# Optimization experiments

Measured on AMD Instinct MI355X. Metric: run time of the kernel, lower is better.

Reference implementation:

```python
import jax, jax.numpy as jnp
import numpy as np

B, C, E, TARGET = 8, 256, 18000, 4500


def setup_inputs() -> dict:
    key = jax.random.key(0)
    k1, k2 = jax.random.split(key)
    fe = jax.random.normal(k1, (B, C, E), dtype=jnp.float32)
    # group_ids[b, e] = index of the pooled output edge that original edge e
    # was merged into by the union-find during edge collapse.
    group_ids = jax.random.randint(k2, (B, E), 0, TARGET, dtype=jnp.int64)
    return {"fe": fe, "group_ids": group_ids, "target": TARGET}


def reference(fe, group_ids, target):
    # MeshUnion.rebuild_features: out feature of each surviving edge group =
    # mean of features of all original edges merged into that group.
    b, c, e = fe.shape
    # flatten (batch, group) into one segment id so a single segment_sum handles all meshes
    flat_ids = (jnp.arange(b, dtype=group_ids.dtype)[:, None] * target + group_ids).reshape(-1)  # [B*E]
    feats = fe.transpose(0, 2, 1).reshape(b * e, c)  # [B*E, C]
    sums = jax.ops.segment_sum(feats, flat_ids, num_segments=b * target)          # [B*T, C]
    counts = jax.ops.segment_sum(jnp.ones((b * e,), fe.dtype), flat_ids,
                                 num_segments=b * target)                          # [B*T]
    out = sums / jnp.maximum(counts, 1.0)[:, None]
    return out.reshape(b, target, c).transpose(0, 2, 1)  # [B, C, target]
```

## Files before the change

kernel.cpp:

```cpp
#include <hip/hip_runtime.h>

#define BB 8
#define CC 256
#define EE 18000
#define TT 4500
#define BT (BB * TT)
#define BE (BB * EE)
#define W  36
#define S  37
#define NW 500
#define PADDED (NW * S)


__global__ void zero_counts_kernel(int* __restrict__ counts) {
    int i = blockIdx.x * blockDim.x + threadIdx.x;
    if (i < BT) counts[i] = 0;
}

__global__ void count_kernel(const int* __restrict__ gid, int* __restrict__ counts) {
    int i = blockIdx.x * blockDim.x + threadIdx.x;
    if (i < BE) {
        int b = i / EE;
        atomicAdd(&counts[b * TT + gid[i]], 1);
    }
}

__global__ __launch_bounds__(1024) void scan_kernel(const int* __restrict__ counts,
                                                    int* __restrict__ cursor,
                                                    unsigned short* __restrict__ pend16,
                                                    float* __restrict__ inv32) {
    __shared__ int part[1024];
    const int b = blockIdx.x;
    const int t = threadIdx.x;
    const int CHUNK = 5;
    int lo = t * CHUNK; if (lo > TT) lo = TT;
    int hi = lo + CHUNK; if (hi > TT) hi = TT;
    int s = 0;
    for (int i = lo; i < hi; ++i) s += counts[b * TT + i];
    part[t] = s;
    __syncthreads();
    for (int d = 1; d < 1024; d <<= 1) {
        int v = (t >= d) ? part[t - d] : 0;
        __syncthreads();
        part[t] += v;
        __syncthreads();
    }
    int run = part[t] - s;
    for (int i = lo; i < hi; ++i) {
        int cnt = counts[b * TT + i];
        cursor[b * TT + i] = b * EE + run;
        int end = run + cnt;
        pend16[b * TT + i] = (end > 0) ? (unsigned short)((end - 1) + (end - 1) / W) : 0;
        inv32[b * TT + i]  = (cnt > 0) ? 1.0f / (float)cnt : 0.0f;
        run = end;
    }
}

__global__ void scatter_kernel(const int* __restrict__ gid,
                               int* __restrict__ cursor,
                               unsigned short* __restrict__ prank16) {
    int i = blockIdx.x * blockDim.x + threadIdx.x;
    if (i < BE) {
        int b = i / EE;
        int p = atomicAdd(&cursor[b * TT + gid[i]], 1) - b * EE;
        prank16[i] = (unsigned short)(p + p / W);
    }
}


__global__ __launch_bounds__(512, 2) void pool_kernel(const float* __restrict__ fe,
                                                      const unsigned short* __restrict__ prank16,
                                                      const unsigned short* __restrict__ pend16,
                                                      const float* __restrict__ inv32,
                                                      float* __restrict__ out) {
    __shared__ float vals[PADDED];
    __shared__ float part[512];
    const int b   = blockIdx.x >> 8;
    const int c   = blockIdx.x & 255;
    const int tid = threadIdx.x;

    if (tid < NW) vals[S * tid + W] = 0.0f;

    const float4*  fe4 = (const float4*)(fe + (size_t)(b * CC + c) * EE);
    const ushort4* rk4 = (const ushort4*)(prank16 + (size_t)b * EE);
#pragma unroll
    for (int i = 0; i < 9; ++i) {
        int idx = tid + (i << 9);
        if (idx < EE / 4) {
            float4  v = fe4[idx];
            ushort4 r = rk4[idx];
            vals[r.x] = v.x;
            vals[r.y] = v.y;
            vals[r.z] = v.z;
            vals[r.w] = v.w;
        }
    }
    __syncthreads();

    float v[W];
    float sum = 0.0f;
    const int base = S * tid;
    if (tid < NW) {
#pragma unroll
        for (int k = 0; k < W; ++k) { v[k] = vals[base + k]; sum += v[k]; }
    }
    part[tid] = sum;
    __syncthreads();

    if (tid < 64) {
        float ps[8];
        float run = 0.0f;
#pragma unroll
        for (int j = 0; j < 8; ++j) { run += part[tid * 8 + j]; ps[j] = run; }
        float tot = run, sc = run;
#pragma unroll
        for (int d = 1; d < 64; d <<= 1) {
            float o = __shfl_up(sc, d, 64);
            if (tid >= d) sc += o;
        }
        float excl = sc - tot;
#pragma unroll
        for (int j = 0; j < 8; ++j) part[tid * 8 + j] = ps[j] + excl;
    }
    __syncthreads();

    if (tid < NW) {
        float run = (tid > 0) ? part[tid - 1] : 0.0f;
#pragma unroll
        for (int k = 0; k < W; ++k) { run += v[k]; vals[base + k] = run; }
    }
    __syncthreads();

    const unsigned short* pe = pend16 + b * TT;
    const float*          iv = inv32 + b * TT;
    float*                outb = out + (size_t)(b * CC + c) * TT;
#pragma unroll
    for (int k = 0; k < 9; ++k) {
        int g = tid + (k << 9);
        if (g < TT) {
            float Pa = vals[pe[g]];
            float Pb = (g > 0) ? vals[pe[g - 1]] : 0.0f;
            outb[g] = (Pa - Pb) * iv[g];
        }
    }
}

extern "C" void kernel_launch(void* const* d_in, const int* in_sizes, int n_in,
                              void* d_out, int out_size, void* d_ws, size_t ws_size,
                              hipStream_t stream) {
    const float* fe  = (const float*)d_in[0];
    const int*   gid = (const int*)d_in[1];
    float*       out = (float*)d_out;

    int*            counts  = (int*)d_ws;
    int*            cursor  = counts + BT;
    float*          inv32   = (float*)(cursor + BT);
    unsigned short* pend16  = (unsigned short*)(inv32 + BT);
    unsigned short* prank16 = pend16 + BT;

    zero_counts_kernel<<<(BT + 255) / 256, 256, 0, stream>>>(counts);
    count_kernel<<<(BE + 255) / 256, 256, 0, stream>>>(gid, counts);
    scan_kernel<<<BB, 1024, 0, stream>>>(counts, cursor, pend16, inv32);
    scatter_kernel<<<(BE + 255) / 256, 256, 0, stream>>>(gid, cursor, prank16);
    pool_kernel<<<BB * CC, 512, 0, stream>>>(fe, prank16, pend16, inv32, out);
}
```

Baseline: 67.02 us.

## Split segment prefix-sum into two halves to halve shared memory per block

Computes a split point per batch at a group boundary near the middle of the sorted edge order. The pool kernel then processes each half separately with a smaller shared prefix buffer and a warp-shuffle block scan. Smaller LDS usage is meant to allow more resident blocks. In exchange, the fe and rank data are read twice per block, and two extra preprocessing kernels are added.

Result: slower. 100.0 us (+49.3%).

```diff
diff --git a/kernel.cpp b/kernel.cpp
--- a/kernel.cpp
+++ b/kernel.cpp
@@ -6,10 +6,11 @@
 #define TT 4500
 #define BT (BB * TT)
 #define BE (BB * EE)
-#define W  36
-#define S  37
-#define NW 500
-#define PADDED (NW * S)
+#define W  18
+#define SS 19
+#define NW 512
+#define PW (NW * SS)
+#define SP 9000
 
 
 __global__ void zero_counts_kernel(int* __restrict__ counts) {
@@ -26,9 +27,8 @@
 }
 
 __global__ __launch_bounds__(1024) void scan_kernel(const int* __restrict__ counts,
-                                                    int* __restrict__ cursor,
-                                                    unsigned short* __restrict__ pend16,
-                                                    float* __restrict__ inv32) {
+                                                    int* __restrict__ off32,
+                                                    int* __restrict__ cursor) {
     __shared__ int part[1024];
     const int b = blockIdx.x;
     const int t = threadIdx.x;
@@ -47,101 +47,136 @@
     }
     int run = part[t] - s;
     for (int i = lo; i < hi; ++i) {
-        int cnt = counts[b * TT + i];
+        off32[b * TT + i]  = run;
         cursor[b * TT + i] = b * EE + run;
-        int end = run + cnt;
-        pend16[b * TT + i] = (end > 0) ? (unsigned short)((end - 1) + (end - 1) / W) : 0;
-        inv32[b * TT + i]  = (cnt > 0) ? 1.0f / (float)cnt : 0.0f;
-        run = end;
+        run += counts[b * TT + i];
+    }
+}
+
+__global__ __launch_bounds__(512) void split_kernel(const int* __restrict__ off32,
+                                                    int2* __restrict__ split2) {
+    const int b = blockIdx.x;
+    for (int g = threadIdx.x; g < TT; g += 512) {
+        int st = off32[b * TT + g];
+        if (st >= SP && g > 0 && off32[b * TT + g - 1] < SP)
+            split2[b] = make_int2(g, st);
+    }
+}
+
+__global__ void table_kernel(const int* __restrict__ counts,
+                             const int* __restrict__ off32,
+                             const int2* __restrict__ split2,
+                             unsigned short* __restrict__ qa16,
+                             unsigned short* __restrict__ qb16,
+                             float* __restrict__ inv32) {
+    int i = blockIdx.x * blockDim.x + threadIdx.x;
+    if (i < BT) {
+        int b = i / TT;
+        int g = i - b * TT;
+        int2 s2 = split2[b];
+        int st  = off32[i];
+        int cnt = counts[i];
+        int ls  = st - ((g >= s2.x) ? s2.y : 0);
+        int le  = ls + cnt;
+        qa16[i] = cnt ? (unsigned short)((le - 1) + (le - 1) / W + 1) : 0;
+        qb16[i] = ls  ? (unsigned short)((ls - 1) + (ls - 1) / W + 1) : 0;
+        inv32[i] = cnt ? 1.0f / (float)cnt : 0.0f;
     }
 }
 
 __global__ void scatter_kernel(const int* __restrict__ gid,
                                int* __restrict__ cursor,
+                               const int2* __restrict__ split2,
                                unsigned short* __restrict__ prank16) {
     int i = blockIdx.x * blockDim.x + threadIdx.x;
     if (i < BE) {
-        int b = i / EE;
-        int p = atomicAdd(&cursor[b * TT + gid[i]], 1) - b * EE;
-        prank16[i] = (unsigned short)(p + p / W);
-    }
-}
-
-
-__global__ __launch_bounds__(512, 2) void pool_kernel(const float* __restrict__ fe,
-                                                      const unsigned short* __restrict__ prank16,
-                                                      const unsigned short* __restrict__ pend16,
-                                                      const float* __restrict__ inv32,
-                                                      float* __restrict__ out) {
-    __shared__ float vals[PADDED];
-    __shared__ float part[512];
+        int b  = i / EE;
+        int p  = atomicAdd(&cursor[b * TT + gid[i]], 1) - b * EE;
+        int sp = split2[b].y;
+        int h  = (p >= sp) ? 1 : 0;
+        int lp = p - (h ? sp : 0);
+        prank16[i] = (unsigned short)((lp + lp / W) | (h << 15));
+    }
+}
+
+
+__global__ __launch_bounds__(512) void pool_kernel(const float* __restrict__ fe,
+                                                   const unsigned short* __restrict__ prank16,
+                                                   const unsigned short* __restrict__ qa16,
+                                                   const unsigned short* __restrict__ qb16,
+                                                   const float* __restrict__ inv32,
+                                                   const int2* __restrict__ split2,
+                                                   float* __restrict__ out) {
+    __shared__ float vals[PW];
+    __shared__ float wsum[8];
     const int b   = blockIdx.x >> 8;
     const int c   = blockIdx.x & 255;
     const int tid = threadIdx.x;
-
-    if (tid < NW) vals[S * tid + W] = 0.0f;
+    const int wv  = tid >> 6;
+    const int ln  = tid & 63;
 
     const float4*  fe4 = (const float4*)(fe + (size_t)(b * CC + c) * EE);
     const ushort4* rk4 = (const ushort4*)(prank16 + (size_t)b * EE);
-#pragma unroll
-    for (int i = 0; i < 9; ++i) {
-        int idx = tid + (i << 9);
-        if (idx < EE / 4) {
-            float4  v = fe4[idx];
-            ushort4 r = rk4[idx];
-            vals[r.x] = v.x;
-            vals[r.y] = v.y;
-            vals[r.z] = v.z;
-            vals[r.w] = v.w;
-        }
-    }
-    __syncthreads();
-
-    float v[W];
-    float sum = 0.0f;
-    const int base = S * tid;
-    if (tid < NW) {
-#pragma unroll
-        for (int k = 0; k < W; ++k) { v[k] = vals[base + k]; sum += v[k]; }
-    }
-    part[tid] = sum;
-    __syncthreads();
-
-    if (tid < 64) {
-        float ps[8];
-        float run = 0.0f;
-#pragma unroll
-        for (int j = 0; j < 8; ++j) { run += part[tid * 8 + j]; ps[j] = run; }
-        float tot = run, sc = run;
+    const unsigned short* qa = qa16 + b * TT;
+    const unsigned short* qb = qb16 + b * TT;
+    const float*          iv = inv32 + b * TT;
+    float* outb = out + (size_t)(b * CC + c) * TT;
+    const int gs = split2[b].x;
+
+    for (int h = 0; h < 2; ++h) {
+        const int hb = h << 15;
+
+        for (int i = tid; i < PW; i += 512) vals[i] = 0.0f;
+        __syncthreads();
+
+#pragma unroll
+        for (int i = 0; i < 9; ++i) {
+            int idx = tid + (i << 9);
+            if (idx < EE / 4) {
+                float4  v = fe4[idx];
+                ushort4 r = rk4[idx];
+                if ((r.x & 0x8000) == hb) vals[r.x & 0x7fff] = v.x;
+                if ((r.y & 0x8000) == hb) vals[r.y & 0x7fff] = v.y;
+                if ((r.z & 0x8000) == hb) vals[r.z & 0x7fff] = v.z;
+                if ((r.w & 0x8000) == hb) vals[r.w & 0x7fff] = v.w;
+            }
+        }
+        __syncthreads();
+
+        const int base = SS * tid;
+        float sum = 0.0f;
+#pragma unroll
+        for (int k = 0; k < W; ++k) sum += vals[base + k];
+
+        float sc = sum;
 #pragma unroll
         for (int d = 1; d < 64; d <<= 1) {
             float o = __shfl_up(sc, d, 64);
-            if (tid >= d) sc += o;
-        }
-        float excl = sc - tot;
-#pragma unroll
-        for (int j = 0; j < 8; ++j) part[tid * 8 + j] = ps[j] + excl;
-    }
-    __syncthreads();
-
-    if (tid < NW) {
-        float run = (tid > 0) ? part[tid - 1] : 0.0f;
-#pragma unroll
-        for (int k = 0; k < W; ++k) { run += v[k]; vals[base + k] = run; }
-    }
-    __syncthreads();
-
-    const unsigned short* pe = pend16 + b * TT;
-    const float*          iv = inv32 + b * TT;
-    float*                outb = out + (size_t)(b * CC + c) * TT;
-#pragma unroll
-    for (int k = 0; k < 9; ++k) {
-        int g = tid + (k << 9);
-        if (g < TT) {
-            float Pa = vals[pe[g]];
-            float Pb = (g > 0) ? vals[pe[g - 1]] : 0.0f;
+            if (ln >= d) sc += o;
+        }
+        if (ln == 63) wsum[wv] = sc;
+        __syncthreads();
+
+        float cross = 0.0f;
+#pragma unroll
+        for (int j = 0; j < 8; ++j) {
+            float tw = wsum[j];
+            if (j < wv) cross += tw;
+        }
+        float run = cross + (sc - sum);
+#pragma unroll
+        for (int k = 0; k < W; ++k) { run += vals[base + k]; vals[base + k] = run; }
+        __syncthreads();
+
+        const int glo = h ? gs : 0;
+        const int ghi = h ? TT : gs;
+        for (int g = glo + tid; g < ghi; g += 512) {
+            int a = qa[g], bq = qb[g];
+            float Pa = a  ? vals[a - 1]  : 0.0f;
+            float Pb = bq ? vals[bq - 1] : 0.0f;
             outb[g] = (Pa - Pb) * iv[g];
         }
+        __syncthreads();
     }
 }
 
@@ -154,13 +189,18 @@
 
     int*            counts  = (int*)d_ws;
     int*            cursor  = counts + BT;
-    float*          inv32   = (float*)(cursor + BT);
-    unsigned short* pend16  = (unsigned short*)(inv32 + BT);
-    unsigned short* prank16 = pend16 + BT;
+    int*            off32   = cursor + BT;
+    float*          inv32   = (float*)(off32 + BT);
+    unsigned short* qa16    = (unsigned short*)(inv32 + BT);
+    unsigned short* qb16    = qa16 + BT;
+    unsigned short* prank16 = qb16 + BT;
+    int2*           split2  = (int2*)(prank16 + BE);
 
     zero_counts_kernel<<<(BT + 255) / 256, 256, 0, stream>>>(counts);
     count_kernel<<<(BE + 255) / 256, 256, 0, stream>>>(gid, counts);
-    scan_kernel<<<BB, 1024, 0, stream>>>(counts, cursor, pend16, inv32);
-    scatter_kernel<<<(BE + 255) / 256, 256, 0, stream>>>(gid, cursor, prank16);
-    pool_kernel<<<BB * CC, 512, 0, stream>>>(fe, prank16, pend16, inv32, out);
-}
+    scan_kernel<<<BB, 1024, 0, stream>>>(counts, off32, cursor);
+    split_kernel<<<BB, 512, 0, stream>>>(off32, split2);
+    table_kernel<<<(BT + 255) / 256, 256, 0, stream>>>(counts, off32, split2, qa16, qb16, inv32);
+    scatter_kernel<<<(BE + 255) / 256, 256, 0, stream>>>(gid, cursor, split2, prank16);
+    pool_kernel<<<BB * CC, 512, 0, stream>>>(fe, prank16, qa16, qb16, inv32, split2, out);
+}
```

## Use 1024-thread pool blocks with wave-shuffle scan and packed index table

Applied to the files above, without the earlier changes.

The pool kernel now runs 1024 threads per block, each handling 18 padded slots instead of 36. The block scan uses per-wave shuffles plus a 16-entry cross-wave sum instead of a serial 64-thread pass. The scan kernel now writes a packed uint2 table holding both prefix endpoints and the reciprocal count. This removes the neighbour pend lookup and one of the separate loads in the output phase. The aim is to keep every thread busy, drop a barrier and cut per-thread register and serial work. The risks are the 1024-thread block shape and an aggressive launch bound that may force register spilling.

New measurement: 65.88 us. No clear change (-1.7%).

```diff
diff --git a/kernel.cpp b/kernel.cpp
--- a/kernel.cpp
+++ b/kernel.cpp
@@ -6,10 +6,10 @@
 #define TT 4500
 #define BT (BB * TT)
 #define BE (BB * EE)
-#define W  36
-#define S  37
-#define NW 500
-#define PADDED (NW * S)
+#define W  18
+#define SS 19
+#define NT 1024
+#define PW (NT * SS)
 
 
 __global__ void zero_counts_kernel(int* __restrict__ counts) {
@@ -27,8 +27,7 @@
 
 __global__ __launch_bounds__(1024) void scan_kernel(const int* __restrict__ counts,
                                                     int* __restrict__ cursor,
-                                                    unsigned short* __restrict__ pend16,
-                                                    float* __restrict__ inv32) {
+                                                    uint2* __restrict__ tab) {
     __shared__ int part[1024];
     const int b = blockIdx.x;
     const int t = threadIdx.x;
@@ -49,10 +48,12 @@
     for (int i = lo; i < hi; ++i) {
         int cnt = counts[b * TT + i];
         cursor[b * TT + i] = b * EE + run;
-        int end = run + cnt;
-        pend16[b * TT + i] = (end > 0) ? (unsigned short)((end - 1) + (end - 1) / W) : 0;
-        inv32[b * TT + i]  = (cnt > 0) ? 1.0f / (float)cnt : 0.0f;
-        run = end;
+        int en = run + cnt;
+        unsigned int qa = cnt ? (unsigned int)((en - 1) + (en - 1) / W + 1) : 0u;
+        unsigned int qb = run ? (unsigned int)((run - 1) + (run - 1) / W + 1) : 0u;
+        float inv = cnt ? 1.0f / (float)cnt : 0.0f;
+        tab[b * TT + i] = make_uint2(qa | (qb << 16), __float_as_uint(inv));
+        run = en;
     }
 }
 
@@ -68,24 +69,23 @@
 }
 
 
-__global__ __launch_bounds__(512, 2) void pool_kernel(const float* __restrict__ fe,
-                                                      const unsigned short* __restrict__ prank16,
-                                                      const unsigned short* __restrict__ pend16,
-                                                      const float* __restrict__ inv32,
-                                                      float* __restrict__ out) {
-    __shared__ float vals[PADDED];
-    __shared__ float part[512];
+__global__ __launch_bounds__(1024, 8) void pool_kernel(const float* __restrict__ fe,
+                                                       const unsigned short* __restrict__ prank16,
+                                                       const uint2* __restrict__ tab,
+                                                       float* __restrict__ out) {
+    __shared__ float vals[PW];
+    __shared__ float wsum[16];
     const int b   = blockIdx.x >> 8;
     const int c   = blockIdx.x & 255;
     const int tid = threadIdx.x;
-
-    if (tid < NW) vals[S * tid + W] = 0.0f;
+    const int wv  = tid >> 6;
+    const int ln  = tid & 63;
 
     const float4*  fe4 = (const float4*)(fe + (size_t)(b * CC + c) * EE);
     const ushort4* rk4 = (const ushort4*)(prank16 + (size_t)b * EE);
 #pragma unroll
-    for (int i = 0; i < 9; ++i) {
-        int idx = tid + (i << 9);
+    for (int i = 0; i < 5; ++i) {
+        int idx = tid + (i << 10);
         if (idx < EE / 4) {
             float4  v = fe4[idx];
             ushort4 r = rk4[idx];
@@ -97,50 +97,51 @@
     }
     __syncthreads();
 
+    const int base = SS * tid;
     float v[W];
-    float sum = 0.0f;
-    const int base = S * tid;
-    if (tid < NW) {
+    float s0 = 0.0f, s1 = 0.0f;
 #pragma unroll
-        for (int k = 0; k < W; ++k) { v[k] = vals[base + k]; sum += v[k]; }
+    for (int k = 0; k < 9; ++k)  { v[k] = vals[base + k]; s0 += v[k]; }
+#pragma unroll
+    for (int k = 9; k < 18; ++k) { v[k] = vals[base + k]; s1 += v[k]; }
+    const float sum = s0 + s1;
+
+    float sc = sum;
+#pragma unroll
+    for (int d = 1; d < 64; d <<= 1) {
+        float o = __shfl_up(sc, d, 64);
+        if (ln >= d) sc += o;
     }
-    part[tid] = sum;
+    if (ln == 63) wsum[wv] = sc;
     __syncthreads();
 
-    if (tid < 64) {
-        float ps[8];
-        float run = 0.0f;
+    float cross = 0.0f;
 #pragma unroll
-        for (int j = 0; j < 8; ++j) { run += part[tid * 8 + j]; ps[j] = run; }
-        float tot = run, sc = run;
+    for (int j = 0; j < 16; ++j) {
+        float tw = wsum[j];
+        if (j < wv) cross += tw;
+    }
+
+    float run0 = cross + (sc - sum);
+    float run1 = run0 + s0;
 #pragma unroll
-        for (int d = 1; d < 64; d <<= 1) {
-            float o = __shfl_up(sc, d, 64);
-            if (tid >= d) sc += o;
-        }
-        float excl = sc - tot;
+    for (int k = 0; k < 9; ++k)  { run0 += v[k]; vals[base + k] = run0; }
 #pragma unroll
-        for (int j = 0; j < 8; ++j) part[tid * 8 + j] = ps[j] + excl;
-    }
+    for (int k = 9; k < 18; ++k) { run1 += v[k]; vals[base + k] = run1; }
     __syncthreads();
 
-    if (tid < NW) {
-        float run = (tid > 0) ? part[tid - 1] : 0.0f;
+    const uint2* tb   = tab + b * TT;
+    float*       outb = out + (size_t)(b * CC + c) * TT;
 #pragma unroll
-        for (int k = 0; k < W; ++k) { run += v[k]; vals[base + k] = run; }
-    }
-    __syncthreads();
-
-    const unsigned short* pe = pend16 + b * TT;
-    const float*          iv = inv32 + b * TT;
-    float*                outb = out + (size_t)(b * CC + c) * TT;
-#pragma unroll
-    for (int k = 0; k < 9; ++k) {
-        int g = tid + (k << 9);
+    for (int k = 0; k < 5; ++k) {
+        int g = tid + (k << 10);
         if (g < TT) {
-            float Pa = vals[pe[g]];
-            float Pb = (g > 0) ? vals[pe[g - 1]] : 0.0f;
-            outb[g] = (Pa - Pb) * iv[g];
+            uint2 q = tb[g];
+            unsigned int a  = q.x & 0xffffu;
+            unsigned int bq = q.x >> 16;
+            float Pa = a  ? vals[a - 1]  : 0.0f;
+            float Pb = bq ? vals[bq - 1] : 0.0f;
+            outb[g] = (Pa - Pb) * __uint_as_float(q.y);
         }
     }
 }
@@ -154,13 +155,12 @@
 
     int*            counts  = (int*)d_ws;
     int*            cursor  = counts + BT;
-    float*          inv32   = (float*)(cursor + BT);
-    unsigned short* pend16  = (unsigned short*)(inv32 + BT);
-    unsigned short* prank16 = pend16 + BT;
+    uint2*          tab     = (uint2*)(cursor + BT);
+    unsigned short* prank16 = (unsigned short*)(tab + BT);
 
     zero_counts_kernel<<<(BT + 255) / 256, 256, 0, stream>>>(counts);
     count_kernel<<<(BE + 255) / 256, 256, 0, stream>>>(gid, counts);
-    scan_kernel<<<BB, 1024, 0, stream>>>(counts, cursor, pend16, inv32);
+    scan_kernel<<<BB, 1024, 0, stream>>>(counts, cursor, tab);
     scatter_kernel<<<(BE + 255) / 256, 256, 0, stream>>>(gid, cursor, prank16);
-    pool_kernel<<<BB * CC, 512, 0, stream>>>(fe, prank16, pend16, inv32, out);
+    pool_kernel<<<BB * CC, 1024, 0, stream>>>(fe, prank16, tab, out);
 }
```
